# Performance work log

Hardware: AMD Instinct MI355X
Metric: run time of the kernel (lower is better)

Reference implementation:

```python
import jax, jax.numpy as jnp
import numpy as np

PATCH = 64      # patch generator patch size
LD = 1.0        # self.ld
WS = 11         # SSIM gaussian window size
SIGMA = 1.5
C1 = 0.01 ** 2
C2 = 0.03 ** 2


def _gauss_window(channels):
    x = jnp.arange(WS, dtype=jnp.float32)
    g = jnp.exp(-((x - WS // 2) ** 2) / (2.0 * SIGMA * SIGMA))
    g = g / g.sum()
    w2 = jnp.outer(g, g)               # (WS, WS), sums to 1
    return jnp.broadcast_to(w2[None, None], (channels, 1, WS, WS))


def _dwconv(x, w, channels):
    # depthwise 'same' conv, padding = WS//2 (matches F.conv2d(..., padding=ws//2, groups=C))
    p = WS // 2
    return jax.lax.conv_general_dilated(
        x, w, window_strides=(1, 1), padding=[(p, p), (p, p)],
        dimension_numbers=("NCHW", "OIHW", "NCHW"), feature_group_count=channels)


def _ssim(img1, img2):
    # img1, img2: (n, C, h, w) -> per-image mean SSIM, shape (n,)
    ch = img1.shape[1]
    w = _gauss_window(ch).astype(img1.dtype)
    mu1 = _dwconv(img1, w, ch)
    mu2 = _dwconv(img2, w, ch)
    mu1_sq, mu2_sq, mu1_mu2 = mu1 * mu1, mu2 * mu2, mu1 * mu2
    sigma1_sq = _dwconv(img1 * img1, w, ch) - mu1_sq
    sigma2_sq = _dwconv(img2 * img2, w, ch) - mu2_sq
    sigma12 = _dwconv(img1 * img2, w, ch) - mu1_mu2
    ssim_map = ((2.0 * mu1_mu2 + C1) * (2.0 * sigma12 + C2)) / (
        (mu1_sq + mu2_sq + C1) * (sigma1_sq + sigma2_sq + C2))
    return jnp.mean(ssim_map, axis=(1, 2, 3))


def _to_patches(x, ps):
    # (B, C, H, W) -> (B, P, C, ps, ps) with P = (H//ps)*(W//ps)
    B, C, H, W = x.shape
    x = x.reshape(B, C, H // ps, ps, W // ps, ps)
    x = x.transpose(0, 2, 4, 1, 3, 5)
    return x.reshape(B, (H // ps) * (W // ps), C, ps, ps)


def setup_inputs() -> dict:
    key = jax.random.key(0)
    ks = jax.random.split(key, 5)
    shp = (32, 3, 512, 512)
    names = ["A", "N", "GT", "G", "BG"]
    return {n: jax.random.uniform(k, shp, dtype=jnp.float32) for n, k in zip(names, ks)}


def reference(A, N, GT, G, BG):
    pA = _to_patches(A, PATCH)
    pN = _to_patches(N, PATCH)
    pGT = _to_patches(GT, PATCH)
    pG = _to_patches(G, PATCH)
    pBG = _to_patches(BG, PATCH)
    B, P, C, h, w = pA.shape
    # batched SSIM over all (B*P) patches (replaces the python double loop)
    ssim_scores = _ssim(pN.reshape(B * P, C, h, w), pGT.reshape(B * P, C, h, w)).reshape(B, P)
    diff = jnp.minimum(LD * (1.0 - ssim_scores), jnp.ones_like(ssim_scores))
    bg_loss = jnp.mean((pBG - pG) ** 2, axis=(2, 3, 4))
    a_loss = jnp.mean((pA - pG) ** 2, axis=(2, 3, 4))
    loss = diff * bg_loss + (1.0 - diff) * a_loss
    return jnp.sum(loss)
```

## Files before the change

### kernel.cpp

```cpp
#include <hip/hip_runtime.h>
#include <math.h>

#define C1C 1e-4f
#define C2C 9e-4f

#define GW0 0.00102838f
#define GW1 0.00759876f
#define GW2 0.03600077f
#define GW3 0.10936069f
#define GW4 0.21300554f
#define GW5 0.26601173f
__device__ __forceinline__ float conv11(const float* w) {
    float a = GW0 * (w[0] + w[10]);
    a = fmaf(GW1, w[1] + w[9], a);
    a = fmaf(GW2, w[2] + w[8], a);
    a = fmaf(GW3, w[3] + w[7], a);
    a = fmaf(GW4, w[4] + w[6], a);
    a = fmaf(GW5, w[5], a);
    return a;
}

__device__ __forceinline__ void load_col26(const float (*S)[68], int col,
                                           int wid, float* w) {
    if (wid == 0) {
        #pragma unroll
        for (int d = 0; d < 5; ++d) w[d] = 0.f;
        #pragma unroll
        for (int d = 5; d < 26; ++d) w[d] = S[d - 5][col];
    } else if (wid == 3) {
        #pragma unroll
        for (int d = 0; d < 21; ++d) w[d] = S[43 + d][col];
        #pragma unroll
        for (int d = 21; d < 26; ++d) w[d] = 0.f;
    } else {
        const int base = (wid << 4) - 5;
        #pragma unroll
        for (int d = 0; d < 26; ++d) w[d] = S[base + d][col];
    }
}

__global__ __launch_bounds__(256, 3) void ssim_fused_kernel(
    const float* __restrict__ A,  const float* __restrict__ Nimg,
    const float* __restrict__ GT, const float* __restrict__ G,
    const float* __restrict__ BG,
    float* __restrict__ ssim_sum, float* __restrict__ sa_sum,
    float* __restrict__ sbg_sum)
{
    __shared__ float S0[64][68];
    __shared__ float S1[64][68];
    __shared__ float S2[64][68];

    const int q  = blockIdx.x;
    const int c  = blockIdx.y;
    const int b  = q >> 6;
    const int pp = q & 63;
    const int ph = pp >> 3;
    const int pw = pp & 7;
    const size_t base = ((size_t)(b * 3 + c) << 18)
                      + ((size_t)(ph * 64) << 9)
                      + (size_t)(pw * 64);
    const int t = threadIdx.x;

    const int hr = t >> 2;
    const int hc = (t & 3) << 4;
    const size_t rowBase = base + ((size_t)hr << 9);

    float hxx[16], hyy[16];

    {
        float xw[32], yw[32];
        #pragma unroll
        for (int m = 0; m < 8; ++m) {
            const int cb = hc - 8 + 4 * m;
            float4 xv = make_float4(0.f, 0.f, 0.f, 0.f);
            float4 yv = make_float4(0.f, 0.f, 0.f, 0.f);
            if (cb >= 0 && cb < 64) {
                xv = *(const float4*)(Nimg + rowBase + cb);
                yv = *(const float4*)(GT   + rowBase + cb);
            }
            xw[4*m+0] = xv.x; xw[4*m+1] = xv.y; xw[4*m+2] = xv.z; xw[4*m+3] = xv.w;
            yw[4*m+0] = yv.x; yw[4*m+1] = yv.y; yw[4*m+2] = yv.z; yw[4*m+3] = yv.w;
        }

        float tp[32];
        #pragma unroll
        for (int i = 0; i < 32; ++i) tp[i] = xw[i] * yw[i];
        #pragma unroll
        for (int m = 0; m < 4; ++m) {
            float4 o0, o1, o2;
            #pragma unroll
            for (int u = 0; u < 4; ++u) {
                const int o = 4 * m + u;
                (&o0.x)[u] = conv11(&xw[o + 3]);
                (&o1.x)[u] = conv11(&yw[o + 3]);
                (&o2.x)[u] = conv11(&tp[o + 3]);
            }
            *(float4*)&S0[hr][hc + 4*m] = o0;
            *(float4*)&S1[hr][hc + 4*m] = o1;
            *(float4*)&S2[hr][hc + 4*m] = o2;
        }
        #pragma unroll
        for (int i = 0; i < 32; ++i) tp[i] = xw[i] * xw[i];
        #pragma unroll
        for (int o = 0; o < 16; ++o) hxx[o] = conv11(&tp[o + 3]);
        #pragma unroll
        for (int i = 0; i < 32; ++i) tp[i] = yw[i] * yw[i];
        #pragma unroll
        for (int o = 0; o < 16; ++o) hyy[o] = conv11(&tp[o + 3]);
    }
    __syncthreads();

    const int vj  = t & 63;
    const int wid = t >> 6;

    float mu1[16], mu2[16], Exy[16];
    {
        float w[26];
        load_col26(S0, vj, wid, w);
        #pragma unroll
        for (int o = 0; o < 16; ++o) mu1[o] = conv11(&w[o]);
        load_col26(S1, vj, wid, w);
        #pragma unroll
        for (int o = 0; o < 16; ++o) mu2[o] = conv11(&w[o]);
        load_col26(S2, vj, wid, w);
        #pragma unroll
        for (int o = 0; o < 16; ++o) Exy[o] = conv11(&w[o]);
    }
    __syncthreads();

    #pragma unroll
    for (int m = 0; m < 4; ++m) {
        float4 o0, o1;
        #pragma unroll
        for (int u = 0; u < 4; ++u) {
            (&o0.x)[u] = hxx[4*m + u];
            (&o1.x)[u] = hyy[4*m + u];
        }
        *(float4*)&S0[hr][hc + 4*m] = o0;
        *(float4*)&S1[hr][hc + 4*m] = o1;
    }
    __syncthreads();

    float accS = 0.f;
    {
        float Exx[16];
        float w[26];
        load_col26(S0, vj, wid, w);
        #pragma unroll
        for (int o = 0; o < 16; ++o) Exx[o] = conv11(&w[o]);
        load_col26(S1, vj, wid, w);
        #pragma unroll
        for (int o = 0; o < 16; ++o) {
            const float Eyy = conv11(&w[o]);
            const float m1 = mu1[o], m2 = mu2[o];
            const float m1s = m1 * m1, m2s = m2 * m2, m12 = m1 * m2;
            const float s1  = Exx[o] - m1s;
            const float s2v = Eyy    - m2s;
            const float s12 = Exy[o] - m12;
            const float num = (2.f * m12 + C1C) * (2.f * s12 + C2C);
            const float den = (m1s + m2s + C1C) * (s1 + s2v + C2C);
            accS += num / den;
        }
    }

    float sa = 0.f, sbg = 0.f;
    #pragma unroll
    for (int it = 0; it < 4; ++it) {
        const int idx  = t + 256 * it;
        const int row  = idx >> 4;
        const int col4 = (idx & 15) << 2;
        const size_t off = base + ((size_t)row << 9) + col4;
        const float4 av  = *(const float4*)(A  + off);
        const float4 gv  = *(const float4*)(G  + off);
        const float4 bgv = *(const float4*)(BG + off);
        float d0 = bgv.x - gv.x, d1 = bgv.y - gv.y, d2 = bgv.z - gv.z, d3 = bgv.w - gv.w;
        sbg += d0*d0 + d1*d1 + d2*d2 + d3*d3;
        float e0 = av.x - gv.x, e1 = av.y - gv.y, e2 = av.z - gv.z, e3 = av.w - gv.w;
        sa  += e0*e0 + e1*e1 + e2*e2 + e3*e3;
    }

    #pragma unroll
    for (int off = 32; off; off >>= 1) {
        accS += __shfl_down(accS, off, 64);
        sa   += __shfl_down(sa,   off, 64);
        sbg  += __shfl_down(sbg,  off, 64);
    }
    __syncthreads();
    if ((t & 63) == 0) {
        S0[0][wid] = accS; S0[1][wid] = sa; S0[2][wid] = sbg;
    }
    __syncthreads();
    if (t == 0) {
        const int plane = q * 3 + c;
        ssim_sum[plane] = S0[0][0] + S0[0][1] + S0[0][2] + S0[0][3];
        sa_sum[plane]   = S0[1][0] + S0[1][1] + S0[1][2] + S0[1][3];
        sbg_sum[plane]  = S0[2][0] + S0[2][1] + S0[2][2] + S0[2][3];
    }
}

__global__ __launch_bounds__(256) void combine_kernel(
    const float* __restrict__ ssim_sum, const float* __restrict__ sa_sum,
    const float* __restrict__ sbg_sum, float* __restrict__ out)
{
    __shared__ float red[4];
    const int t = threadIdx.x;
    const float invN = 1.f / 12288.f;
    float acc = 0.f;
    #pragma unroll
    for (int r = 0; r < 8; ++r) {
        const int qq = t + 256 * r;
        const float ss = ssim_sum[3*qq] + ssim_sum[3*qq+1] + ssim_sum[3*qq+2];
        const float sa = sa_sum[3*qq]   + sa_sum[3*qq+1]   + sa_sum[3*qq+2];
        const float sb = sbg_sum[3*qq]  + sbg_sum[3*qq+1]  + sbg_sum[3*qq+2];
        const float ssim = ss * invN;
        const float diff = fminf(1.f - ssim, 1.f);
        acc += diff * (sb * invN) + (1.f - diff) * (sa * invN);
    }
    #pragma unroll
    for (int off = 32; off; off >>= 1) acc += __shfl_down(acc, off, 64);
    if ((t & 63) == 0) red[t >> 6] = acc;
    __syncthreads();
    if (t == 0) out[0] = red[0] + red[1] + red[2] + red[3];
}

extern "C" void kernel_launch(void* const* d_in, const int* in_sizes, int n_in,
                              void* d_out, int out_size, void* d_ws, size_t ws_size,
                              hipStream_t stream) {
    const float* A  = (const float*)d_in[0];
    const float* Nn = (const float*)d_in[1];
    const float* GT = (const float*)d_in[2];
    const float* G  = (const float*)d_in[3];
    const float* BG = (const float*)d_in[4];
    float* out      = (float*)d_out;

    float* ssim_sum = (float*)d_ws;
    float* sa_sum   = ssim_sum + 6144;
    float* sbg_sum  = ssim_sum + 12288;

    ssim_fused_kernel<<<dim3(2048, 3), 256, 0, stream>>>(
        A, Nn, GT, G, BG, ssim_sum, sa_sum, sbg_sum);
    combine_kernel<<<1, 256, 0, stream>>>(ssim_sum, sa_sum, sbg_sum, out);
}
```

Before: 434.4 us.

## Split SSIM patch into two column halves with zero-padded smaller shared tiles

Processes each 64x64 patch in two 32-column halves. Each half uses shared tiles of 74 rows by 36 columns, with zeroed halo rows so the vertical pass no longer needs per-wave boundary branches. Per-thread register arrays and LDS footprint shrink, which allows a launch bound of 5 blocks per SM instead of 3 and is meant to raise occupancy. In exchange, each block runs twice as many barriers and horizontal halo loads, and adds a zero-initialisation loop.

```diff
diff --git a/kernel.cpp b/kernel.cpp
--- a/kernel.cpp
+++ b/kernel.cpp
@@ -20,35 +20,19 @@
     return a;
 }
 
-__device__ __forceinline__ void load_col26(const float (*S)[68], int col,
-                                           int wid, float* w) {
-    if (wid == 0) {
-        #pragma unroll
-        for (int d = 0; d < 5; ++d) w[d] = 0.f;
-        #pragma unroll
-        for (int d = 5; d < 26; ++d) w[d] = S[d - 5][col];
-    } else if (wid == 3) {
-        #pragma unroll
-        for (int d = 0; d < 21; ++d) w[d] = S[43 + d][col];
-        #pragma unroll
-        for (int d = 21; d < 26; ++d) w[d] = 0.f;
-    } else {
-        const int base = (wid << 4) - 5;
-        #pragma unroll
-        for (int d = 0; d < 26; ++d) w[d] = S[base + d][col];
-    }
-}
-
-__global__ __launch_bounds__(256, 3) void ssim_fused_kernel(
+#define SROWS 74
+#define SSTR  36
+
+__global__ __launch_bounds__(256, 5) void ssim_fused_kernel(
     const float* __restrict__ A,  const float* __restrict__ Nimg,
     const float* __restrict__ GT, const float* __restrict__ G,
     const float* __restrict__ BG,
     float* __restrict__ ssim_sum, float* __restrict__ sa_sum,
     float* __restrict__ sbg_sum)
 {
-    __shared__ float S0[64][68];
-    __shared__ float S1[64][68];
-    __shared__ float S2[64][68];
+    __shared__ float S0[SROWS][SSTR];
+    __shared__ float S1[SROWS][SSTR];
+    __shared__ float S2[SROWS][SSTR];
 
     const int q  = blockIdx.x;
     const int c  = blockIdx.y;
@@ -61,17 +45,28 @@
                       + (size_t)(pw * 64);
     const int t = threadIdx.x;
 
-    const int hr = t >> 2;
-    const int hc = (t & 3) << 4;
+    for (int i = t; i < 10 * SSTR; i += 256) {
+        const int r  = i / SSTR;
+        const int cc = i - r * SSTR;
+        const int rr = (r < 5) ? r : 64 + r;
+        S0[rr][cc] = 0.f; S1[rr][cc] = 0.f; S2[rr][cc] = 0.f;
+    }
+
+    const int hr   = t >> 2;
+    const int hseg = t & 3;
+    const int c0   = hseg << 3;
     const size_t rowBase = base + ((size_t)hr << 9);
-
-    float hxx[16], hyy[16];
-
-    {
-        float xw[32], yw[32];
+    const int vcol = t & 31;
+    const int vr0  = (t >> 5) << 3;
+
+    float accS = 0.f;
+
+    for (int h = 0; h < 2; ++h) {
+        const int g0 = (h << 5) + c0;
+        float xw[24], yw[24];
         #pragma unroll
-        for (int m = 0; m < 8; ++m) {
-            const int cb = hc - 8 + 4 * m;
+        for (int m = 0; m < 6; ++m) {
+            const int cb = g0 - 8 + 4 * m;
             float4 xv = make_float4(0.f, 0.f, 0.f, 0.f);
             float4 yv = make_float4(0.f, 0.f, 0.f, 0.f);
             if (cb >= 0 && cb < 64) {
@@ -82,85 +77,97 @@
             yw[4*m+0] = yv.x; yw[4*m+1] = yv.y; yw[4*m+2] = yv.z; yw[4*m+3] = yv.w;
         }
 
-        float tp[32];
+        float hx[8], hy[8];
+        {
+            float tp[24];
+            #pragma unroll
+            for (int i = 0; i < 24; ++i) tp[i] = xw[i] * yw[i];
+            #pragma unroll
+            for (int mm = 0; mm < 2; ++mm) {
+                float4 o;
+                #pragma unroll
+                for (int u = 0; u < 4; ++u) (&o.x)[u] = conv11(&tp[4*mm + u + 3]);
+                *(float4*)&S2[5 + hr][c0 + 4*mm] = o;
+            }
+            #pragma unroll
+            for (int i = 0; i < 24; ++i) tp[i] = xw[i] * xw[i];
+            #pragma unroll
+            for (int mm = 0; mm < 2; ++mm) {
+                float4 o;
+                #pragma unroll
+                for (int u = 0; u < 4; ++u) (&o.x)[u] = conv11(&tp[4*mm + u + 3]);
+                *(float4*)&S0[5 + hr][c0 + 4*mm] = o;
+            }
+            #pragma unroll
+            for (int i = 0; i < 24; ++i) tp[i] = yw[i] * yw[i];
+            #pragma unroll
+            for (int mm = 0; mm < 2; ++mm) {
+                float4 o;
+                #pragma unroll
+                for (int u = 0; u < 4; ++u) (&o.x)[u] = conv11(&tp[4*mm + u + 3]);
+                *(float4*)&S1[5 + hr][c0 + 4*mm] = o;
+            }
+            #pragma unroll
+            for (int o = 0; o < 8; ++o) hx[o] = conv11(&xw[o + 3]);
+            #pragma unroll
+            for (int o = 0; o < 8; ++o) hy[o] = conv11(&yw[o + 3]);
+        }
+        __syncthreads();
+
+        float Exx[8], Eyy[8], Exy[8];
+        {
+            float w[18];
+            #pragma unroll
+            for (int d = 0; d < 18; ++d) w[d] = S0[vr0 + d][vcol];
+            #pragma unroll
+            for (int o = 0; o < 8; ++o) Exx[o] = conv11(&w[o]);
+            #pragma unroll
+            for (int d = 0; d < 18; ++d) w[d] = S1[vr0 + d][vcol];
+            #pragma unroll
+            for (int o = 0; o < 8; ++o) Eyy[o] = conv11(&w[o]);
+            #pragma unroll
+            for (int d = 0; d < 18; ++d) w[d] = S2[vr0 + d][vcol];
+            #pragma unroll
+            for (int o = 0; o < 8; ++o) Exy[o] = conv11(&w[o]);
+        }
+        __syncthreads();
+
         #pragma unroll
-        for (int i = 0; i < 32; ++i) tp[i] = xw[i] * yw[i];
-        #pragma unroll
-        for (int m = 0; m < 4; ++m) {
-            float4 o0, o1, o2;
+        for (int mm = 0; mm < 2; ++mm) {
+            float4 o0, o1;
             #pragma unroll
             for (int u = 0; u < 4; ++u) {
-                const int o = 4 * m + u;
-                (&o0.x)[u] = conv11(&xw[o + 3]);
-                (&o1.x)[u] = conv11(&yw[o + 3]);
-                (&o2.x)[u] = conv11(&tp[o + 3]);
-            }
-            *(float4*)&S0[hr][hc + 4*m] = o0;
-            *(float4*)&S1[hr][hc + 4*m] = o1;
-            *(float4*)&S2[hr][hc + 4*m] = o2;
-        }
-        #pragma unroll
-        for (int i = 0; i < 32; ++i) tp[i] = xw[i] * xw[i];
-        #pragma unroll
-        for (int o = 0; o < 16; ++o) hxx[o] = conv11(&tp[o + 3]);
-        #pragma unroll
-        for (int i = 0; i < 32; ++i) tp[i] = yw[i] * yw[i];
-        #pragma unroll
-        for (int o = 0; o < 16; ++o) hyy[o] = conv11(&tp[o + 3]);
-    }
-    __syncthreads();
-
-    const int vj  = t & 63;
-    const int wid = t >> 6;
-
-    float mu1[16], mu2[16], Exy[16];
-    {
-        float w[26];
-        load_col26(S0, vj, wid, w);
-        #pragma unroll
-        for (int o = 0; o < 16; ++o) mu1[o] = conv11(&w[o]);
-        load_col26(S1, vj, wid, w);
-        #pragma unroll
-        for (int o = 0; o < 16; ++o) mu2[o] = conv11(&w[o]);
-        load_col26(S2, vj, wid, w);
-        #pragma unroll
-        for (int o = 0; o < 16; ++o) Exy[o] = conv11(&w[o]);
-    }
-    __syncthreads();
-
-    #pragma unroll
-    for (int m = 0; m < 4; ++m) {
-        float4 o0, o1;
-        #pragma unroll
-        for (int u = 0; u < 4; ++u) {
-            (&o0.x)[u] = hxx[4*m + u];
-            (&o1.x)[u] = hyy[4*m + u];
-        }
-        *(float4*)&S0[hr][hc + 4*m] = o0;
-        *(float4*)&S1[hr][hc + 4*m] = o1;
-    }
-    __syncthreads();
-
-    float accS = 0.f;
-    {
-        float Exx[16];
-        float w[26];
-        load_col26(S0, vj, wid, w);
-        #pragma unroll
-        for (int o = 0; o < 16; ++o) Exx[o] = conv11(&w[o]);
-        load_col26(S1, vj, wid, w);
-        #pragma unroll
-        for (int o = 0; o < 16; ++o) {
-            const float Eyy = conv11(&w[o]);
-            const float m1 = mu1[o], m2 = mu2[o];
-            const float m1s = m1 * m1, m2s = m2 * m2, m12 = m1 * m2;
-            const float s1  = Exx[o] - m1s;
-            const float s2v = Eyy    - m2s;
-            const float s12 = Exy[o] - m12;
-            const float num = (2.f * m12 + C1C) * (2.f * s12 + C2C);
-            const float den = (m1s + m2s + C1C) * (s1 + s2v + C2C);
-            accS += num / den;
-        }
+                (&o0.x)[u] = hx[4*mm + u];
+                (&o1.x)[u] = hy[4*mm + u];
+            }
+            *(float4*)&S0[5 + hr][c0 + 4*mm] = o0;
+            *(float4*)&S1[5 + hr][c0 + 4*mm] = o1;
+        }
+        __syncthreads();
+
+        {
+            float w[18];
+            #pragma unroll
+            for (int d = 0; d < 18; ++d) w[d] = S0[vr0 + d][vcol];
+            float mu1[8];
+            #pragma unroll
+            for (int o = 0; o < 8; ++o) mu1[o] = conv11(&w[o]);
+            #pragma unroll
+            for (int d = 0; d < 18; ++d) w[d] = S1[vr0 + d][vcol];
+            #pragma unroll
+            for (int o = 0; o < 8; ++o) {
+                const float m2  = conv11(&w[o]);
+                const float m1  = mu1[o];
+                const float m1s = m1 * m1, m2s = m2 * m2, m12 = m1 * m2;
+                const float s1  = Exx[o] - m1s;
+                const float s2v = Eyy[o] - m2s;
+                const float s12 = Exy[o] - m12;
+                const float num = (2.f * m12 + C1C) * (2.f * s12 + C2C);
+                const float den = (m1s + m2s + C1C) * (s1 + s2v + C2C);
+                accS += num / den;
+            }
+        }
+        __syncthreads();
     }
 
     float sa = 0.f, sbg = 0.f;
@@ -185,9 +192,9 @@
         sa   += __shfl_down(sa,   off, 64);
         sbg  += __shfl_down(sbg,  off, 64);
     }
-    __syncthreads();
+    const int wv = t >> 6;
     if ((t & 63) == 0) {
-        S0[0][wid] = accS; S0[1][wid] = sa; S0[2][wid] = sbg;
+        S0[0][wv] = accS; S0[1][wv] = sa; S0[2][wv] = sbg;
     }
     __syncthreads();
     if (t == 0) {
```

Measured after the change: 717.9 us. 65.3% more time.
